# Optimization experiments

Measured on AMD Instinct MI355X. Metric: run time of the kernel, lower is better.

Reference implementation:

```python
import jax, jax.numpy as jnp
import numpy as np

B, S, D, H, OUT = 512, 200, 64, 512, 1
EPS = 1e-5  # torch LayerNorm default


def ln(x, g, b, axes=-1):
    m = x.mean(axis=axes, keepdims=True)
    v = ((x - m) ** 2).mean(axis=axes, keepdims=True)
    return (x - m) * jax.lax.rsqrt(v + EPS) * g + b


def lstm_layer(xs, W_ih, b_ih, W_hh, b_hh, g_ih, be_ih, g_hh, be_hh, g_ho, be_ho):
    # xs: (S, B, in_dim) -> (S, B, H)
    nb = xs.shape[1]
    def step(carry, x_t):
        h, c = carry
        gates = ln(x_t @ W_ih.T + b_ih, g_ih, be_ih) + ln(h @ W_hh.T + b_hh, g_hh, be_hh)
        i, f, g, o = jnp.split(gates, 4, axis=-1)
        c_new = jax.nn.sigmoid(f) * c + jax.nn.sigmoid(i) * jnp.tanh(g)
        h_new = jax.nn.sigmoid(o) * ln(jnp.tanh(c_new), g_ho, be_ho)
        return (h_new, c_new), h_new
    init = (jnp.zeros((nb, H), xs.dtype), jnp.zeros((nb, H), xs.dtype))
    _, hs = jax.lax.scan(step, init, xs)
    return hs


def setup_inputs() -> dict:
    key = jax.random.key(0)
    ks = iter(jax.random.split(key, 16))
    scale = 0.02
    def rn(shape):
        return jax.random.normal(next(ks), shape, jnp.float32) * scale
    inp = {"x": jax.random.normal(next(ks), (B, S, D), jnp.float32)}
    inp["ln1_g"] = jnp.ones((S, D), jnp.float32)
    inp["ln1_b"] = jnp.zeros((S, D), jnp.float32)
    for l, ind in ((0, D), (1, H)):
        inp[f"W_ih{l}"] = rn((4 * H, ind)); inp[f"b_ih{l}"] = jnp.zeros((4 * H,), jnp.float32)
        inp[f"W_hh{l}"] = rn((4 * H, H));  inp[f"b_hh{l}"] = jnp.zeros((4 * H,), jnp.float32)
        inp[f"g_ih{l}"] = jnp.ones((4 * H,), jnp.float32); inp[f"be_ih{l}"] = jnp.zeros((4 * H,), jnp.float32)
        inp[f"g_hh{l}"] = jnp.ones((4 * H,), jnp.float32); inp[f"be_hh{l}"] = jnp.zeros((4 * H,), jnp.float32)
        inp[f"g_ho{l}"] = jnp.ones((H,), jnp.float32);     inp[f"be_ho{l}"] = jnp.zeros((H,), jnp.float32)
    inp["Wd1"] = rn((H // 4, H));      inp["bd1"] = jnp.zeros((H // 4,), jnp.float32)
    inp["Wd2"] = rn((H // 8, H // 4)); inp["bd2"] = jnp.zeros((H // 8,), jnp.float32)
    inp["Wd3"] = rn((H // 16, H // 8)); inp["bd3"] = jnp.zeros((H // 16,), jnp.float32)
    inp["Wd4"] = rn((OUT, H // 16));   inp["bd4"] = jnp.zeros((OUT,), jnp.float32)
    return inp


def _forward(x, ln1_g, ln1_b,
             W_ih0, b_ih0, W_hh0, b_hh0, g_ih0, be_ih0, g_hh0, be_hh0, g_ho0, be_ho0,
             W_ih1, b_ih1, W_hh1, b_hh1, g_ih1, be_ih1, g_hh1, be_hh1, g_ho1, be_ho1,
             Wd1, bd1, Wd2, bd2, Wd3, bd3, Wd4, bd4):
    # ln1 normalizes jointly over (seq_len, input_dim)
    x = ln(x, ln1_g, ln1_b, axes=(-2, -1))
    xs = jnp.transpose(x, (1, 0, 2))  # (S, B, D)
    hs = lstm_layer(xs, W_ih0, b_ih0, W_hh0, b_hh0, g_ih0, be_ih0, g_hh0, be_hh0, g_ho0, be_ho0)
    hs = lstm_layer(hs, W_ih1, b_ih1, W_hh1, b_hh1, g_ih1, be_ih1, g_hh1, be_hh1, g_ho1, be_ho1)
    h_last = hs[-1]  # (B, H): last_num=1, eval-mode dropout is identity
    z = jax.nn.relu(h_last @ Wd1.T + bd1)
    z = jax.nn.relu(z @ Wd2.T + bd2)
    z = jax.nn.relu(z @ Wd3.T + bd3)
    return z @ Wd4.T + bd4  # (B, OUT)


def reference(x, ln1_g, ln1_b,
              W_ih0, b_ih0, W_hh0, b_hh0, g_ih0, be_ih0, g_hh0, be_hh0, g_ho0, be_ho0,
              W_ih1, b_ih1, W_hh1, b_hh1, g_ih1, be_ih1, g_hh1, be_hh1, g_ho1, be_ho1,
              Wd1, bd1, Wd2, bd2, Wd3, bd3, Wd4, bd4):
    return _forward(x, ln1_g, ln1_b,
                    W_ih0, b_ih0, W_hh0, b_hh0, g_ih0, be_ih0, g_hh0, be_hh0, g_ho0, be_ho0,
                    W_ih1, b_ih1, W_hh1, b_hh1, g_ih1, be_ih1, g_hh1, be_hh1, g_ho1, be_ho1,
                    Wd1, bd1, Wd2, bd2, Wd3, bd3, Wd4, bd4)
```

## Files before the change

kernel.cpp:

```cpp
#include <hip/hip_runtime.h>
#include <math.h>

#define BATCH 512
#define SEQ   200
#define DIN   64
#define HID   512
#define GW    2048
#define EPS   1e-5f
#define NREG  4

typedef _Float16 half_t;
typedef half_t half8 __attribute__((ext_vector_type(8)));
typedef float  f32x4  __attribute__((ext_vector_type(4)));
typedef float  f32x16 __attribute__((ext_vector_type(16)));

#define WN0 (2048*64)
#define WN1 (2048*512)
#define WTOT (WN0 + 3*WN1)
#define XFRAG ((size_t)SEQ*16*4*512)

__device__ __forceinline__ float sigf(float x){ return 1.0f/(1.0f+expf(-x)); }

__device__ __forceinline__ void gload16(const half_t* g, half_t* l){
  __builtin_amdgcn_global_load_lds(
      (const __attribute__((address_space(1))) void*)g,
      (__attribute__((address_space(3))) void*)l, 16, 0, 0);
}

__device__ __forceinline__ void barf(){
  asm volatile("" ::: "memory");
  __builtin_amdgcn_s_barrier();
  asm volatile("" ::: "memory");
}

__device__ __forceinline__ void block_reduce4(float&a,float&b,float&c,float&d,float* red){
  #pragma unroll
  for(int o=32;o;o>>=1){
    a+=__shfl_down(a,o); b+=__shfl_down(b,o);
    c+=__shfl_down(c,o); d+=__shfl_down(d,o);
  }
  const int lane = threadIdx.x & 63, wid = threadIdx.x>>6;
  if(lane==0){ red[wid*4+0]=a; red[wid*4+1]=b; red[wid*4+2]=c; red[wid*4+3]=d; }
  __syncthreads();
  a = red[0]+red[4]+red[8]+red[12];
  b = red[1]+red[5]+red[9]+red[13];
  c = red[2]+red[6]+red[10]+red[14];
  d = red[3]+red[7]+red[11]+red[15];
  __syncthreads();
}

__global__ __launch_bounds__(256) void ln1_stats(const float* __restrict__ x,
                                                 float* __restrict__ mu,
                                                 float* __restrict__ rs){
  const int b = blockIdx.x;
  const float* xb = x + (size_t)b*SEQ*DIN;
  float s=0, ss=0, d=0, e=0;
  for (int i=threadIdx.x; i<SEQ*DIN; i+=256){ float v=xb[i]; s+=v; ss+=v*v; }
  __shared__ float red[16];
  block_reduce4(s,ss,d,e,red);
  if (threadIdx.x==0){
    float m = s*(1.0f/(SEQ*DIN));
    mu[b] = m;
    rs[b] = rsqrtf(ss*(1.0f/(SEQ*DIN)) - m*m + EPS);
  }
}

__global__ __launch_bounds__(256) void wsplit(
    const float* __restrict__ W0, const float* __restrict__ W1,
    const float* __restrict__ W2, const float* __restrict__ W3,
    half_t* __restrict__ Wh, half_t* __restrict__ Wl)
{
  int i = blockIdx.x*256 + threadIdx.x;
  if (i >= WTOT) return;
  const float* src; int off, Kd;
  if (i < WN0){ src=W0; off=i; Kd=DIN; }
  else {
    int r = (i-WN0)/WN1; off = (i-WN0) - r*WN1; Kd=HID;
    src = (r==0)?W1:((r==1)?W2:W3);
  }
  const int C = Kd>>5;
  int j  = off & 7;
  int l  = (off>>3) & 63;
  int ks = (off>>9) & 1;
  int nf = (off>>10) & 1;
  int pc = off>>11;
  int c  = pc & (C-1);
  int p  = pc >> (Kd==DIN ? 1 : 4);
  int n  = p*64 + nf*32 + (l&31);
  int k  = c*32 + ks*16 + (l>>5)*8 + j;
  float v = src[(size_t)n*Kd + k];
  half_t h = (half_t)v;
  Wh[i] = h;
  Wl[i] = (half_t)(v - (float)h);
}

__global__ __launch_bounds__(256) void xprep(
    const float* __restrict__ x, const float* __restrict__ g1, const float* __restrict__ b1,
    const float* __restrict__ mu, const float* __restrict__ rs,
    half_t* __restrict__ xh, half_t* __restrict__ xl)
{
  size_t i = (size_t)blockIdx.x*256 + threadIdx.x;
  if (i >= XFRAG) return;
  int j   = (int)(i & 7);
  int l   = (int)((i>>3) & 63);
  int c   = (int)((i>>9) & 3);
  int mch = (int)((i>>11) & 15);
  int t   = (int)(i>>15);
  int b   = mch*32 + (l&31);
  int k   = c*16 + ((l>>5)<<3) + j;
  float v = (x[(size_t)b*(SEQ*DIN) + t*DIN + k] - mu[b]) * rs[b]
            * g1[t*DIN+k] + b1[t*DIN+k];
  half_t h = (half_t)v;
  xh[i] = h;
  xl[i] = (half_t)(v - (float)h);
}

__global__ __launch_bounds__(256, 1) void tick_mm64(
    const half_t* __restrict__ xh, const half_t* __restrict__ xl,
    const half_t* __restrict__ h0fh, const half_t* __restrict__ h0fl,
    const half_t* __restrict__ h1fh, const half_t* __restrict__ h1fl,
    const half_t* __restrict__ Wh, const half_t* __restrict__ Wl,
    float* __restrict__ G, int t)
{
  __shared__ half_t sbuf[2*16384];

  const int bi   = blockIdx.x;
  const int xcd  = bi & 7;
  const int slot = bi >> 3;
  const int z    = slot & 3;
  const int y    = (slot >> 2) & 3;
  const int x    = xcd*2 + (slot >> 4);

  const int tid  = threadIdx.x;
  const int lane = tid & 63;
  const int w    = tid >> 6;
  const int ln31 = lane & 31;

  const int mch0 = y*4 + (w>>1)*2;
  const int p    = x*2 + (w&1);
  const int wn0  = p*64;

  const half_t* BHb = Wh + WN0; const half_t* BLb = Wl + WN0;
  int Kd = HID;
  if (z==0){ BHb=Wh; BLb=Wl; Kd=DIN; }
  else if (z==2){ BHb=Wh+WN0+WN1; BLb=Wl+WN0+WN1; }
  else if (z==3){ BHb=Wh+WN0+2*WN1; BLb=Wl+WN0+2*WN1; }

  const int C32 = Kd >> 5;
  const int C16 = Kd >> 4;

  const int tq = (t < SEQ) ? t : (SEQ-1);
  const half_t *AHb, *ALb;
  if (z==0){ AHb = xh + (size_t)tq*32768; ALb = xl + (size_t)tq*32768; }
  else if (z==3){ AHb = h1fh; ALb = h1fl; }
  else { AHb = h0fh; ALb = h0fl; }

  auto stage = [&](int s){
    half_t* dst = sbuf + (size_t)(s&1)*16384;
    if (w < 2){
      #pragma unroll
      for (int q=0;q<2;q++){
        const int mci = w*2+q;
        const size_t abase = ((size_t)(y*4+mci)*C16 + 2*s)*512;
        #pragma unroll
        for (int pl=0;pl<2;pl++){
          const half_t* src = (pl? ALb : AHb) + abase + lane*8;
          half_t* d = dst + (mci*2+pl)*1024;
          gload16(src,       d);
          gload16(src + 512, d + 512);
        }
      }
    } else {
      const int ph = w-2;
      const size_t bbase = ((size_t)(x*2+ph)*C32 + s)*2048;
      #pragma unroll
      for (int pl=0;pl<2;pl++){
        const half_t* src = (pl? BLb : BHb) + bbase + lane*8;
        half_t* d = dst + 8192 + (ph*2+pl)*2048;
        #pragma unroll
        for (int i=0;i<4;i++)
          gload16(src + i*512, d + i*512);
      }
    }
  };

  f32x16 acc00 = {0.f,0.f,0.f,0.f,0.f,0.f,0.f,0.f,0.f,0.f,0.f,0.f,0.f,0.f,0.f,0.f};
  f32x16 acc01 = acc00, acc10 = acc00, acc11 = acc00;

  const int mh = w>>1, pw = w&1;
  auto compute = [&](const half_t* buf, int ks){
    const half_t* Ab = buf;
    const half_t* Bb = buf + 8192;
    half8 ah0 = *(const half8*)(Ab + ((mh*2+0)*2+0)*1024 + ks*512 + lane*8);
    half8 al0 = *(const half8*)(Ab + ((mh*2+0)*2+1)*1024 + ks*512 + lane*8);
    half8 ah1 = *(const half8*)(Ab + ((mh*2+1)*2+0)*1024 + ks*512 + lane*8);
    half8 al1 = *(const half8*)(Ab + ((mh*2+1)*2+1)*1024 + ks*512 + lane*8);
    half8 bh0 = *(const half8*)(Bb + ((pw*2+0)*4 + 0 + ks)*512 + lane*8);
    half8 bh1 = *(const half8*)(Bb + ((pw*2+0)*4 + 2 + ks)*512 + lane*8);
    half8 bl0 = *(const half8*)(Bb + ((pw*2+1)*4 + 0 + ks)*512 + lane*8);
    half8 bl1 = *(const half8*)(Bb + ((pw*2+1)*4 + 2 + ks)*512 + lane*8);
    acc00 = __builtin_amdgcn_mfma_f32_32x32x16_f16(ah0, bh0, acc00, 0,0,0);
    acc01 = __builtin_amdgcn_mfma_f32_32x32x16_f16(ah0, bh1, acc01, 0,0,0);
    acc10 = __builtin_amdgcn_mfma_f32_32x32x16_f16(ah1, bh0, acc10, 0,0,0);
    acc11 = __builtin_amdgcn_mfma_f32_32x32x16_f16(ah1, bh1, acc11, 0,0,0);
    acc00 = __builtin_amdgcn_mfma_f32_32x32x16_f16(al0, bh0, acc00, 0,0,0);
    acc01 = __builtin_amdgcn_mfma_f32_32x32x16_f16(al0, bh1, acc01, 0,0,0);
    acc10 = __builtin_amdgcn_mfma_f32_32x32x16_f16(al1, bh0, acc10, 0,0,0);
    acc11 = __builtin_amdgcn_mfma_f32_32x32x16_f16(al1, bh1, acc11, 0,0,0);
    acc00 = __builtin_amdgcn_mfma_f32_32x32x16_f16(ah0, bl0, acc00, 0,0,0);
    acc01 = __builtin_amdgcn_mfma_f32_32x32x16_f16(ah0, bl1, acc01, 0,0,0);
    acc10 = __builtin_amdgcn_mfma_f32_32x32x16_f16(ah1, bl0, acc10, 0,0,0);
    acc11 = __builtin_amdgcn_mfma_f32_32x32x16_f16(ah1, bl1, acc11, 0,0,0);
  };

  stage(0);
  for (int s=0; s<C32; ++s){
    if (s+1 < C32){
      stage(s+1);
      asm volatile("s_waitcnt vmcnt(8)" ::: "memory");
    } else {
      asm volatile("s_waitcnt vmcnt(0)" ::: "memory");
    }
    __builtin_amdgcn_sched_barrier(0);
    barf();
    const half_t* buf = sbuf + (size_t)(s&1)*16384;
    compute(buf, 0);
    compute(buf, 1);
    barf();
  }

  float* Gr = G + (size_t)z*BATCH*GW;
  const int rbase = (lane>>5)<<2;
  #pragma unroll
  for (int reg=0; reg<16; reg++){
    const int row = (reg&3) + ((reg>>2)<<3) + rbase;
    const int m0 = mch0*32 + row;
    const int m1 = m0 + 32;
    __builtin_nontemporal_store(acc00[reg], &Gr[(size_t)m0*GW + wn0 + ln31]);
    __builtin_nontemporal_store(acc01[reg], &Gr[(size_t)m0*GW + wn0 + 32 + ln31]);
    __builtin_nontemporal_store(acc10[reg], &Gr[(size_t)m1*GW + wn0 + ln31]);
    __builtin_nontemporal_store(acc11[reg], &Gr[(size_t)m1*GW + wn0 + 32 + ln31]);
  }
}

__global__ __launch_bounds__(256) void tick_update(
    const float* __restrict__ G,
    const float* __restrict__ b_ih0, const float* __restrict__ b_hh0,
    const float* __restrict__ b_ih1, const float* __restrict__ b_hh1,
    const float* __restrict__ g_ih0, const float* __restrict__ be_ih0,
    const float* __restrict__ g_hh0, const float* __restrict__ be_hh0,
    const float* __restrict__ g_ho0, const float* __restrict__ be_ho0,
    const float* __restrict__ g_ih1, const float* __restrict__ be_ih1,
    const float* __restrict__ g_hh1, const float* __restrict__ be_hh1,
    const float* __restrict__ g_ho1, const float* __restrict__ be_ho1,
    float* __restrict__ h0, float* __restrict__ c0,
    float* __restrict__ h1, float* __restrict__ c1,
    half_t* __restrict__ h0fh, half_t* __restrict__ h0fl,
    half_t* __restrict__ h1fh, half_t* __restrict__ h1fl, int t)
{
  const int layer = blockIdx.x >> 9;
  const int b = blockIdx.x & 511;
  if (layer==0 && t>=SEQ) return;
  if (layer==1 && t==0)   return;

  const float *GA,*GB,*bA,*bB,*gA,*beA,*gB,*beB,*gH,*bH;
  float *cs,*hs; half_t *hfx,*lfx;
  const size_t rb = (size_t)b*GW;
  if (layer==0){
    GA = G + rb;
    GB = G + (size_t)1*BATCH*GW + rb;
    bA=b_ih0; bB=b_hh0;
    gA=g_ih0; beA=be_ih0; gB=g_hh0; beB=be_hh0; gH=g_ho0; bH=be_ho0;
    cs = c0 + b*HID; hs = nullptr; hfx = h0fh; lfx = h0fl;
  } else {
    GA = G + (size_t)2*BATCH*GW + rb;
    GB = G + (size_t)3*BATCH*GW + rb;
    bA=b_ih1; bB=b_hh1;
    gA=g_ih1; beA=be_ih1; gB=g_hh1; beB=be_hh1; gH=g_ho1; bH=be_ho1;
    cs = c1 + b*HID; hs = (t==SEQ) ? (h1 + b*HID) : nullptr; hfx = h1fh; lfx = h1fl;
  }

  const int tid = threadIdx.x;
  __shared__ float red[16];
  __shared__ __align__(16) float GS[2*GW];
  __shared__ float su[HID];
  __shared__ float so[HID];

  float sa=0, ssa=0, sb=0, ssb=0;
  for (int i=tid*4; i<GW; i+=1024){
    f32x4 va = __builtin_nontemporal_load((const f32x4*)(GA+i));
    va += *(const f32x4*)(bA+i);
    *(f32x4*)(GS+i) = va;
    f32x4 vb = __builtin_nontemporal_load((const f32x4*)(GB+i));
    vb += *(const f32x4*)(bB+i);
    *(f32x4*)(GS+GW+i) = vb;
    #pragma unroll
    for (int q=0;q<4;q++){
      sa += va[q]; ssa += va[q]*va[q];
      sb += vb[q]; ssb += vb[q]*vb[q];
    }
  }
  block_reduce4(sa,ssa,sb,ssb,red);
  const float ma = sa*(1.0f/GW);
  const float ra = rsqrtf(ssa*(1.0f/GW) - ma*ma + EPS);
  const float mb = sb*(1.0f/GW);
  const float rb_ = rsqrtf(ssb*(1.0f/GW) - mb*mb + EPS);

  float s_u=0, s_uu=0;
  for (int j=tid;j<HID;j+=256){
    float iv = ((GS[j      ]-ma)*ra*gA[j      ]+beA[j      ]) + ((GS[GW+j      ]-mb)*rb_*gB[j      ]+beB[j      ]);
    float fv = ((GS[j+  HID]-ma)*ra*gA[j+  HID]+beA[j+  HID]) + ((GS[GW+j+  HID]-mb)*rb_*gB[j+  HID]+beB[j+  HID]);
    float gv = ((GS[j+2*HID]-ma)*ra*gA[j+2*HID]+beA[j+2*HID]) + ((GS[GW+j+2*HID]-mb)*rb_*gB[j+2*HID]+beB[j+2*HID]);
    float ov = ((GS[j+3*HID]-ma)*ra*gA[j+3*HID]+beA[j+3*HID]) + ((GS[GW+j+3*HID]-mb)*rb_*gB[j+3*HID]+beB[j+3*HID]);
    float cn = sigf(fv)*cs[j] + sigf(iv)*tanhf(gv);
    cs[j] = cn;
    float u = tanhf(cn);
    su[j] = u; so[j] = sigf(ov);
    s_u += u; s_uu += u*u;
  }
  float d3=0,d4=0;
  block_reduce4(s_u,s_uu,d3,d4,red);
  const float mu_u = s_u*(1.0f/HID);
  const float ru   = rsqrtf(s_uu*(1.0f/HID) - mu_u*mu_u + EPS);

  const size_t fbase = ((size_t)(b>>5)*32)*512 + (size_t)(b&31)*8;
  for (int j=tid;j<HID;j+=256){
    float v = so[j] * ((su[j]-mu_u)*ru*gH[j] + bH[j]);
    if (hs) hs[j] = v;
    half_t hv = (half_t)v;
    half_t lv = (half_t)(v - (float)hv);
    const size_t fi = fbase + (size_t)(j>>4)*512 + (size_t)((j>>3)&1)*256 + (j&7);
    hfx[fi] = hv;
    lfx[fi] = lv;
  }
}

__global__ __launch_bounds__(256) void head_kernel(
    const float* __restrict__ h1,
    const float* __restrict__ Wd1, const float* __restrict__ bd1,
    const float* __restrict__ Wd2, const float* __restrict__ bd2,
    const float* __restrict__ Wd3, const float* __restrict__ bd3,
    const float* __restrict__ Wd4, const float* __restrict__ bd4,
    float* __restrict__ out)
{
  const int b = blockIdx.x;
  __shared__ float hv[HID];
  __shared__ float z1[128];
  __shared__ float z2[64];
  __shared__ float z3[32];
  const int tid = threadIdx.x;
  for (int i=tid;i<HID;i+=256) hv[i]=h1[(size_t)b*HID+i];
  __syncthreads();
  if (tid<128){
    float acc=bd1[tid]; const float* w=Wd1+(size_t)tid*512;
    for(int k=0;k<512;k++) acc+=hv[k]*w[k];
    z1[tid]=fmaxf(acc,0.f);
  }
  __syncthreads();
  if (tid<64){
    float acc=bd2[tid]; const float* w=Wd2+(size_t)tid*128;
    for(int k=0;k<128;k++) acc+=z1[k]*w[k];
    z2[tid]=fmaxf(acc,0.f);
  }
  __syncthreads();
  if (tid<32){
    float acc=bd3[tid]; const float* w=Wd3+(size_t)tid*64;
    for(int k=0;k<64;k++) acc+=z2[k]*w[k];
    z3[tid]=fmaxf(acc,0.f);
  }
  __syncthreads();
  if (tid==0){
    float acc=bd4[0];
    for(int k=0;k<32;k++) acc+=z3[k]*Wd4[k];
    out[b]=acc;
  }
}

extern "C" void kernel_launch(void* const* d_in, const int* in_sizes, int n_in,
                              void* d_out, int out_size, void* d_ws, size_t ws_size,
                              hipStream_t stream) {
  const float* x      = (const float*)d_in[0];
  const float* ln1_g  = (const float*)d_in[1];
  const float* ln1_b  = (const float*)d_in[2];
  const float* W_ih0  = (const float*)d_in[3];
  const float* b_ih0  = (const float*)d_in[4];
  const float* W_hh0  = (const float*)d_in[5];
  const float* b_hh0  = (const float*)d_in[6];
  const float* g_ih0  = (const float*)d_in[7];
  const float* be_ih0 = (const float*)d_in[8];
  const float* g_hh0  = (const float*)d_in[9];
  const float* be_hh0 = (const float*)d_in[10];
  const float* g_ho0  = (const float*)d_in[11];
  const float* be_ho0 = (const float*)d_in[12];
  const float* W_ih1  = (const float*)d_in[13];
  const float* b_ih1  = (const float*)d_in[14];
  const float* W_hh1  = (const float*)d_in[15];
  const float* b_hh1  = (const float*)d_in[16];
  const float* g_ih1  = (const float*)d_in[17];
  const float* be_ih1 = (const float*)d_in[18];
  const float* g_hh1  = (const float*)d_in[19];
  const float* be_hh1 = (const float*)d_in[20];
  const float* g_ho1  = (const float*)d_in[21];
  const float* be_ho1 = (const float*)d_in[22];
  const float* Wd1    = (const float*)d_in[23];
  const float* bd1    = (const float*)d_in[24];
  const float* Wd2    = (const float*)d_in[25];
  const float* bd2    = (const float*)d_in[26];
  const float* Wd3    = (const float*)d_in[27];
  const float* bd3    = (const float*)d_in[28];
  const float* Wd4    = (const float*)d_in[29];
  const float* bd4    = (const float*)d_in[30];
  float* out = (float*)d_out;

  float* ws = (float*)d_ws;
  float* G  = ws;
  float* h0 = G  + NREG*(size_t)BATCH*GW;
  float* c0 = h0 + (size_t)BATCH*HID;
  float* h1 = c0 + (size_t)BATCH*HID;
  float* c1 = h1 + (size_t)BATCH*HID;
  half_t* h0fh = (half_t*)(c1 + (size_t)BATCH*HID);
  half_t* h0fl = h0fh + (size_t)BATCH*HID;
  half_t* h1fh = h0fl + (size_t)BATCH*HID;
  half_t* h1fl = h1fh + (size_t)BATCH*HID;
  float* mu = (float*)(h1fl + (size_t)BATCH*HID);
  float* rs = mu + BATCH;
  half_t* Wh = (half_t*)(rs + BATCH);
  half_t* Wl = Wh + (size_t)WTOT;
  half_t* xh = Wl + (size_t)WTOT;
  half_t* xl = xh + XFRAG;

  (void)hipMemsetAsync(h0, 0, 4*(size_t)BATCH*HID*4 + 4*(size_t)BATCH*HID*2, stream);

  ln1_stats<<<BATCH, 256, 0, stream>>>(x, mu, rs);
  wsplit<<<(WTOT+255)/256, 256, 0, stream>>>(W_ih0, W_hh0, W_ih1, W_hh1, Wh, Wl);
  xprep<<<(int)((XFRAG+255)/256), 256, 0, stream>>>(x, ln1_g, ln1_b, mu, rs, xh, xl);

  for (int t = 0; t <= SEQ; ++t) {
    tick_mm64<<<dim3(256), 256, 0, stream>>>(xh, xl,
        h0fh, h0fl, h1fh, h1fl, Wh, Wl, G, t);
    tick_update<<<dim3(1024), 256, 0, stream>>>(G,
        b_ih0, b_hh0, b_ih1, b_hh1,
        g_ih0, be_ih0, g_hh0, be_hh0, g_ho0, be_ho0,
        g_ih1, be_ih1, g_hh1, be_hh1, g_ho1, be_ho1,
        h0, c0, h1, c1, h0fh, h0fl, h1fh, h1fl, t);
  }
  head_kernel<<<BATCH, 256, 0, stream>>>(h1, Wd1, bd1, Wd2, bd2, Wd3, bd3, Wd4, bd4, out);
}
```

Before: 5.498 ms.

## Split K dimension of recurrent GEMMs across blocks and sum partials in update

The per-step GEMM kernel now launches 448 blocks instead of 256, giving each K=512 GEMM two blocks that each cover half of K, with the x-projection handled by a single block. The partial results go to seven separate G planes and the update kernel adds the two halves while loading them. Launch bounds are raised to allow two blocks per CU. The intent is to spread the short-K recurrent matmul across more CUs and cut per-step latency, at the cost of extra G memory traffic and an extra add in the update kernel.

Result: slower. 5.937 ms (+8.0%).

```diff
diff --git a/kernel.cpp b/kernel.cpp
--- a/kernel.cpp
+++ b/kernel.cpp
@@ -7,7 +7,7 @@
 #define HID   512
 #define GW    2048
 #define EPS   1e-5f
-#define NREG  4
+#define NREG  7
 
 typedef _Float16 half_t;
 typedef half_t half8 __attribute__((ext_vector_type(8)));
@@ -115,7 +115,7 @@
   xl[i] = (half_t)(v - (float)h);
 }
 
-__global__ __launch_bounds__(256, 1) void tick_mm64(
+__global__ __launch_bounds__(256, 2) void tick_mm64(
     const half_t* __restrict__ xh, const half_t* __restrict__ xl,
     const half_t* __restrict__ h0fh, const half_t* __restrict__ h0fl,
     const half_t* __restrict__ h1fh, const half_t* __restrict__ h1fl,
@@ -124,12 +124,13 @@
 {
   __shared__ half_t sbuf[2*16384];
 
-  const int bi   = blockIdx.x;
-  const int xcd  = bi & 7;
-  const int slot = bi >> 3;
-  const int z    = slot & 3;
-  const int y    = (slot >> 2) & 3;
-  const int x    = xcd*2 + (slot >> 4);
+  const int bi    = blockIdx.x;
+  const int zz    = bi >> 6;
+  const int which = (zz+1) >> 1;
+  const int kb    = zz ? ((zz-1)&1)*8 : 0;
+  const int ii    = bi & 63;
+  const int y     = ii & 3;
+  const int x     = ii >> 2;
 
   const int tid  = threadIdx.x;
   const int lane = tid & 63;
@@ -142,17 +143,18 @@
 
   const half_t* BHb = Wh + WN0; const half_t* BLb = Wl + WN0;
   int Kd = HID;
-  if (z==0){ BHb=Wh; BLb=Wl; Kd=DIN; }
-  else if (z==2){ BHb=Wh+WN0+WN1; BLb=Wl+WN0+WN1; }
-  else if (z==3){ BHb=Wh+WN0+2*WN1; BLb=Wl+WN0+2*WN1; }
-
-  const int C32 = Kd >> 5;
-  const int C16 = Kd >> 4;
+  if (which==0){ BHb=Wh; BLb=Wl; Kd=DIN; }
+  else if (which==2){ BHb=Wh+WN0+WN1; BLb=Wl+WN0+WN1; }
+  else if (which==3){ BHb=Wh+WN0+2*WN1; BLb=Wl+WN0+2*WN1; }
+
+  const int C32f = Kd >> 5;
+  const int C16f = Kd >> 4;
+  const int Cloc = (which==0) ? 2 : 8;
 
   const int tq = (t < SEQ) ? t : (SEQ-1);
   const half_t *AHb, *ALb;
-  if (z==0){ AHb = xh + (size_t)tq*32768; ALb = xl + (size_t)tq*32768; }
-  else if (z==3){ AHb = h1fh; ALb = h1fl; }
+  if (which==0){ AHb = xh + (size_t)tq*32768; ALb = xl + (size_t)tq*32768; }
+  else if (which==3){ AHb = h1fh; ALb = h1fl; }
   else { AHb = h0fh; ALb = h0fl; }
 
   auto stage = [&](int s){
@@ -161,7 +163,7 @@
       #pragma unroll
       for (int q=0;q<2;q++){
         const int mci = w*2+q;
-        const size_t abase = ((size_t)(y*4+mci)*C16 + 2*s)*512;
+        const size_t abase = ((size_t)(y*4+mci)*C16f + 2*(kb+s))*512;
         #pragma unroll
         for (int pl=0;pl<2;pl++){
           const half_t* src = (pl? ALb : AHb) + abase + lane*8;
@@ -172,7 +174,7 @@
       }
     } else {
       const int ph = w-2;
-      const size_t bbase = ((size_t)(x*2+ph)*C32 + s)*2048;
+      const size_t bbase = ((size_t)(x*2+ph)*C32f + kb + s)*2048;
       #pragma unroll
       for (int pl=0;pl<2;pl++){
         const half_t* src = (pl? BLb : BHb) + bbase + lane*8;
@@ -214,8 +216,8 @@
   };
 
   stage(0);
-  for (int s=0; s<C32; ++s){
-    if (s+1 < C32){
+  for (int s=0; s<Cloc; ++s){
+    if (s+1 < Cloc){
       stage(s+1);
       asm volatile("s_waitcnt vmcnt(8)" ::: "memory");
     } else {
@@ -229,7 +231,7 @@
     barf();
   }
 
-  float* Gr = G + (size_t)z*BATCH*GW;
+  float* Gr = G + (size_t)zz*BATCH*GW;
   const int rbase = (lane>>5)<<2;
   #pragma unroll
   for (int reg=0; reg<16; reg++){
@@ -263,18 +265,18 @@
   if (layer==0 && t>=SEQ) return;
   if (layer==1 && t==0)   return;
 
-  const float *GA,*GB,*bA,*bB,*gA,*beA,*gB,*beB,*gH,*bH;
+  const float *GA0,*GA1,*GB0,*GB1,*bA,*bB,*gA,*beA,*gB,*beB,*gH,*bH;
   float *cs,*hs; half_t *hfx,*lfx;
   const size_t rb = (size_t)b*GW;
   if (layer==0){
-    GA = G + rb;
-    GB = G + (size_t)1*BATCH*GW + rb;
+    GA0 = G + rb;                        GA1 = nullptr;
+    GB0 = G + (size_t)1*BATCH*GW + rb;   GB1 = G + (size_t)2*BATCH*GW + rb;
     bA=b_ih0; bB=b_hh0;
     gA=g_ih0; beA=be_ih0; gB=g_hh0; beB=be_hh0; gH=g_ho0; bH=be_ho0;
     cs = c0 + b*HID; hs = nullptr; hfx = h0fh; lfx = h0fl;
   } else {
-    GA = G + (size_t)2*BATCH*GW + rb;
-    GB = G + (size_t)3*BATCH*GW + rb;
+    GA0 = G + (size_t)3*BATCH*GW + rb;   GA1 = G + (size_t)4*BATCH*GW + rb;
+    GB0 = G + (size_t)5*BATCH*GW + rb;   GB1 = G + (size_t)6*BATCH*GW + rb;
     bA=b_ih1; bB=b_hh1;
     gA=g_ih1; beA=be_ih1; gB=g_hh1; beB=be_hh1; gH=g_ho1; bH=be_ho1;
     cs = c1 + b*HID; hs = (t==SEQ) ? (h1 + b*HID) : nullptr; hfx = h1fh; lfx = h1fl;
@@ -288,10 +290,12 @@
 
   float sa=0, ssa=0, sb=0, ssb=0;
   for (int i=tid*4; i<GW; i+=1024){
-    f32x4 va = __builtin_nontemporal_load((const f32x4*)(GA+i));
+    f32x4 va = __builtin_nontemporal_load((const f32x4*)(GA0+i));
+    if (GA1) va += __builtin_nontemporal_load((const f32x4*)(GA1+i));
     va += *(const f32x4*)(bA+i);
     *(f32x4*)(GS+i) = va;
-    f32x4 vb = __builtin_nontemporal_load((const f32x4*)(GB+i));
+    f32x4 vb = __builtin_nontemporal_load((const f32x4*)(GB0+i));
+    vb += __builtin_nontemporal_load((const f32x4*)(GB1+i));
     vb += *(const f32x4*)(bB+i);
     *(f32x4*)(GS+GW+i) = vb;
     #pragma unroll
@@ -436,7 +440,7 @@
   xprep<<<(int)((XFRAG+255)/256), 256, 0, stream>>>(x, ln1_g, ln1_b, mu, rs, xh, xl);
 
   for (int t = 0; t <= SEQ; ++t) {
-    tick_mm64<<<dim3(256), 256, 0, stream>>>(xh, xl,
+    tick_mm64<<<dim3(448), 256, 0, stream>>>(xh, xl,
         h0fh, h0fl, h1fh, h1fl, Wh, Wl, G, t);
     tick_update<<<dim3(1024), 256, 0, stream>>>(G,
         b_ih0, b_hh0, b_ih1, b_hh1,
```

## Fuse per-tick matmul and LSTM update into one kernel with grid barrier

Applied to the files above, without the earlier changes.

Merges the per-timestep MFMA gate matmul kernel and the LayerNorm/LSTM cell update kernel into a single launch. An atomic counter per tick acts as a grid-wide barrier between the two phases, which relies on all 256 blocks being co-resident. The update phase is remapped so each wave handles one (layer, batch) row, using wave shuffles instead of block reductions and reusing the matmul LDS buffer. This removes one kernel launch and its drain gap per timestep. The cost is a spin-wait barrier and only 1024 waves doing the elementwise update, far less parallelism than the previous 1024 blocks of 256 threads.

Measured after the change: 20.03 ms. 264% more time.

```diff
diff --git a/kernel.cpp b/kernel.cpp
--- a/kernel.cpp
+++ b/kernel.cpp
@@ -8,6 +8,7 @@
 #define GW    2048
 #define EPS   1e-5f
 #define NREG  4
+#define NBLK_MM 256
 
 typedef _Float16 half_t;
 typedef half_t half8 __attribute__((ext_vector_type(8)));
@@ -31,6 +32,18 @@
   asm volatile("" ::: "memory");
   __builtin_amdgcn_s_barrier();
   asm volatile("" ::: "memory");
+}
+
+__device__ __forceinline__ void wred2(float&a,float&b){
+  #pragma unroll
+  for(int o=32;o;o>>=1){ a+=__shfl_xor(a,o); b+=__shfl_xor(b,o); }
+}
+__device__ __forceinline__ void wred4(float&a,float&b,float&c,float&d){
+  #pragma unroll
+  for(int o=32;o;o>>=1){
+    a+=__shfl_xor(a,o); b+=__shfl_xor(b,o);
+    c+=__shfl_xor(c,o); d+=__shfl_xor(d,o);
+  }
 }
 
 __device__ __forceinline__ void block_reduce4(float&a,float&b,float&c,float&d,float* red){
@@ -115,136 +128,12 @@
   xl[i] = (half_t)(v - (float)h);
 }
 
-__global__ __launch_bounds__(256, 1) void tick_mm64(
+__global__ __launch_bounds__(256, 1) void tick_fused(
     const half_t* __restrict__ xh, const half_t* __restrict__ xl,
-    const half_t* __restrict__ h0fh, const half_t* __restrict__ h0fl,
-    const half_t* __restrict__ h1fh, const half_t* __restrict__ h1fl,
+    half_t* __restrict__ h0fh, half_t* __restrict__ h0fl,
+    half_t* __restrict__ h1fh, half_t* __restrict__ h1fl,
     const half_t* __restrict__ Wh, const half_t* __restrict__ Wl,
-    float* __restrict__ G, int t)
-{
-  __shared__ half_t sbuf[2*16384];
-
-  const int bi   = blockIdx.x;
-  const int xcd  = bi & 7;
-  const int slot = bi >> 3;
-  const int z    = slot & 3;
-  const int y    = (slot >> 2) & 3;
-  const int x    = xcd*2 + (slot >> 4);
-
-  const int tid  = threadIdx.x;
-  const int lane = tid & 63;
-  const int w    = tid >> 6;
-  const int ln31 = lane & 31;
-
-  const int mch0 = y*4 + (w>>1)*2;
-  const int p    = x*2 + (w&1);
-  const int wn0  = p*64;
-
-  const half_t* BHb = Wh + WN0; const half_t* BLb = Wl + WN0;
-  int Kd = HID;
-  if (z==0){ BHb=Wh; BLb=Wl; Kd=DIN; }
-  else if (z==2){ BHb=Wh+WN0+WN1; BLb=Wl+WN0+WN1; }
-  else if (z==3){ BHb=Wh+WN0+2*WN1; BLb=Wl+WN0+2*WN1; }
-
-  const int C32 = Kd >> 5;
-  const int C16 = Kd >> 4;
-
-  const int tq = (t < SEQ) ? t : (SEQ-1);
-  const half_t *AHb, *ALb;
-  if (z==0){ AHb = xh + (size_t)tq*32768; ALb = xl + (size_t)tq*32768; }
-  else if (z==3){ AHb = h1fh; ALb = h1fl; }
-  else { AHb = h0fh; ALb = h0fl; }
-
-  auto stage = [&](int s){
-    half_t* dst = sbuf + (size_t)(s&1)*16384;
-    if (w < 2){
-      #pragma unroll
-      for (int q=0;q<2;q++){
-        const int mci = w*2+q;
-        const size_t abase = ((size_t)(y*4+mci)*C16 + 2*s)*512;
-        #pragma unroll
-        for (int pl=0;pl<2;pl++){
-          const half_t* src = (pl? ALb : AHb) + abase + lane*8;
-          half_t* d = dst + (mci*2+pl)*1024;
-          gload16(src,       d);
-          gload16(src + 512, d + 512);
-        }
-      }
-    } else {
-      const int ph = w-2;
-      const size_t bbase = ((size_t)(x*2+ph)*C32 + s)*2048;
-      #pragma unroll
-      for (int pl=0;pl<2;pl++){
-        const half_t* src = (pl? BLb : BHb) + bbase + lane*8;
-        half_t* d = dst + 8192 + (ph*2+pl)*2048;
-        #pragma unroll
-        for (int i=0;i<4;i++)
-          gload16(src + i*512, d + i*512);
-      }
-    }
-  };
-
-  f32x16 acc00 = {0.f,0.f,0.f,0.f,0.f,0.f,0.f,0.f,0.f,0.f,0.f,0.f,0.f,0.f,0.f,0.f};
-  f32x16 acc01 = acc00, acc10 = acc00, acc11 = acc00;
-
-  const int mh = w>>1, pw = w&1;
-  auto compute = [&](const half_t* buf, int ks){
-    const half_t* Ab = buf;
-    const half_t* Bb = buf + 8192;
-    half8 ah0 = *(const half8*)(Ab + ((mh*2+0)*2+0)*1024 + ks*512 + lane*8);
-    half8 al0 = *(const half8*)(Ab + ((mh*2+0)*2+1)*1024 + ks*512 + lane*8);
-    half8 ah1 = *(const half8*)(Ab + ((mh*2+1)*2+0)*1024 + ks*512 + lane*8);
-    half8 al1 = *(const half8*)(Ab + ((mh*2+1)*2+1)*1024 + ks*512 + lane*8);
-    half8 bh0 = *(const half8*)(Bb + ((pw*2+0)*4 + 0 + ks)*512 + lane*8);
-    half8 bh1 = *(const half8*)(Bb + ((pw*2+0)*4 + 2 + ks)*512 + lane*8);
-    half8 bl0 = *(const half8*)(Bb + ((pw*2+1)*4 + 0 + ks)*512 + lane*8);
-    half8 bl1 = *(const half8*)(Bb + ((pw*2+1)*4 + 2 + ks)*512 + lane*8);
-    acc00 = __builtin_amdgcn_mfma_f32_32x32x16_f16(ah0, bh0, acc00, 0,0,0);
-    acc01 = __builtin_amdgcn_mfma_f32_32x32x16_f16(ah0, bh1, acc01, 0,0,0);
-    acc10 = __builtin_amdgcn_mfma_f32_32x32x16_f16(ah1, bh0, acc10, 0,0,0);
-    acc11 = __builtin_amdgcn_mfma_f32_32x32x16_f16(ah1, bh1, acc11, 0,0,0);
-    acc00 = __builtin_amdgcn_mfma_f32_32x32x16_f16(al0, bh0, acc00, 0,0,0);
-    acc01 = __builtin_amdgcn_mfma_f32_32x32x16_f16(al0, bh1, acc01, 0,0,0);
-    acc10 = __builtin_amdgcn_mfma_f32_32x32x16_f16(al1, bh0, acc10, 0,0,0);
-    acc11 = __builtin_amdgcn_mfma_f32_32x32x16_f16(al1, bh1, acc11, 0,0,0);
-    acc00 = __builtin_amdgcn_mfma_f32_32x32x16_f16(ah0, bl0, acc00, 0,0,0);
-    acc01 = __builtin_amdgcn_mfma_f32_32x32x16_f16(ah0, bl1, acc01, 0,0,0);
-    acc10 = __builtin_amdgcn_mfma_f32_32x32x16_f16(ah1, bl0, acc10, 0,0,0);
-    acc11 = __builtin_amdgcn_mfma_f32_32x32x16_f16(ah1, bl1, acc11, 0,0,0);
-  };
-
-  stage(0);
-  for (int s=0; s<C32; ++s){
-    if (s+1 < C32){
-      stage(s+1);
-      asm volatile("s_waitcnt vmcnt(8)" ::: "memory");
-    } else {
-      asm volatile("s_waitcnt vmcnt(0)" ::: "memory");
-    }
-    __builtin_amdgcn_sched_barrier(0);
-    barf();
-    const half_t* buf = sbuf + (size_t)(s&1)*16384;
-    compute(buf, 0);
-    compute(buf, 1);
-    barf();
-  }
-
-  float* Gr = G + (size_t)z*BATCH*GW;
-  const int rbase = (lane>>5)<<2;
-  #pragma unroll
-  for (int reg=0; reg<16; reg++){
-    const int row = (reg&3) + ((reg>>2)<<3) + rbase;
-    const int m0 = mch0*32 + row;
-    const int m1 = m0 + 32;
-    __builtin_nontemporal_store(acc00[reg], &Gr[(size_t)m0*GW + wn0 + ln31]);
-    __builtin_nontemporal_store(acc01[reg], &Gr[(size_t)m0*GW + wn0 + 32 + ln31]);
-    __builtin_nontemporal_store(acc10[reg], &Gr[(size_t)m1*GW + wn0 + ln31]);
-    __builtin_nontemporal_store(acc11[reg], &Gr[(size_t)m1*GW + wn0 + 32 + ln31]);
-  }
-}
-
-__global__ __launch_bounds__(256) void tick_update(
-    const float* __restrict__ G,
+    float* __restrict__ G, int* __restrict__ ctr,
     const float* __restrict__ b_ih0, const float* __restrict__ b_hh0,
     const float* __restrict__ b_ih1, const float* __restrict__ b_hh1,
     const float* __restrict__ g_ih0, const float* __restrict__ be_ih0,
@@ -253,85 +142,219 @@
     const float* __restrict__ g_ih1, const float* __restrict__ be_ih1,
     const float* __restrict__ g_hh1, const float* __restrict__ be_hh1,
     const float* __restrict__ g_ho1, const float* __restrict__ be_ho1,
-    float* __restrict__ h0, float* __restrict__ c0,
-    float* __restrict__ h1, float* __restrict__ c1,
-    half_t* __restrict__ h0fh, half_t* __restrict__ h0fl,
-    half_t* __restrict__ h1fh, half_t* __restrict__ h1fl, int t)
+    float* __restrict__ c0, float* __restrict__ c1, float* __restrict__ h1,
+    int t)
 {
-  const int layer = blockIdx.x >> 9;
-  const int b = blockIdx.x & 511;
-  if (layer==0 && t>=SEQ) return;
-  if (layer==1 && t==0)   return;
-
-  const float *GA,*GB,*bA,*bB,*gA,*beA,*gB,*beB,*gH,*bH;
-  float *cs,*hs; half_t *hfx,*lfx;
-  const size_t rb = (size_t)b*GW;
-  if (layer==0){
-    GA = G + rb;
-    GB = G + (size_t)1*BATCH*GW + rb;
-    bA=b_ih0; bB=b_hh0;
-    gA=g_ih0; beA=be_ih0; gB=g_hh0; beB=be_hh0; gH=g_ho0; bH=be_ho0;
-    cs = c0 + b*HID; hs = nullptr; hfx = h0fh; lfx = h0fl;
-  } else {
-    GA = G + (size_t)2*BATCH*GW + rb;
-    GB = G + (size_t)3*BATCH*GW + rb;
-    bA=b_ih1; bB=b_hh1;
-    gA=g_ih1; beA=be_ih1; gB=g_hh1; beB=be_hh1; gH=g_ho1; bH=be_ho1;
-    cs = c1 + b*HID; hs = (t==SEQ) ? (h1 + b*HID) : nullptr; hfx = h1fh; lfx = h1fl;
-  }
-
-  const int tid = threadIdx.x;
-  __shared__ float red[16];
-  __shared__ __align__(16) float GS[2*GW];
-  __shared__ float su[HID];
-  __shared__ float so[HID];
-
-  float sa=0, ssa=0, sb=0, ssb=0;
-  for (int i=tid*4; i<GW; i+=1024){
-    f32x4 va = __builtin_nontemporal_load((const f32x4*)(GA+i));
-    va += *(const f32x4*)(bA+i);
-    *(f32x4*)(GS+i) = va;
-    f32x4 vb = __builtin_nontemporal_load((const f32x4*)(GB+i));
-    vb += *(const f32x4*)(bB+i);
-    *(f32x4*)(GS+GW+i) = vb;
+  __shared__ __align__(16) half_t sbuf[2*16384];
+
+  const int bi   = blockIdx.x;
+  const int tid  = threadIdx.x;
+  const int lane = tid & 63;
+  const int w    = tid >> 6;
+  const int ln31 = lane & 31;
+
+  {
+    const int slot = bi >> 3;
+    const int z    = slot & 3;
+    const int y    = (slot >> 2) & 3;
+    const int x    = (bi & 7)*2 + (slot >> 4);
+
+    const int mch0 = y*4 + (w>>1)*2;
+    const int p    = x*2 + (w&1);
+    const int wn0  = p*64;
+
+    const half_t* BHb = Wh + WN0; const half_t* BLb = Wl + WN0;
+    int Kd = HID;
+    if (z==0){ BHb=Wh; BLb=Wl; Kd=DIN; }
+    else if (z==2){ BHb=Wh+WN0+WN1; BLb=Wl+WN0+WN1; }
+    else if (z==3){ BHb=Wh+WN0+2*WN1; BLb=Wl+WN0+2*WN1; }
+
+    const int C32 = Kd >> 5;
+    const int C16 = Kd >> 4;
+
+    const int tq = (t < SEQ) ? t : (SEQ-1);
+    const half_t *AHb, *ALb;
+    if (z==0){ AHb = xh + (size_t)tq*32768; ALb = xl + (size_t)tq*32768; }
+    else if (z==3){ AHb = h1fh; ALb = h1fl; }
+    else { AHb = h0fh; ALb = h0fl; }
+
+    auto stage = [&](int s){
+      half_t* dst = sbuf + (size_t)(s&1)*16384;
+      if (w < 2){
+        #pragma unroll
+        for (int q=0;q<2;q++){
+          const int mci = w*2+q;
+          const size_t abase = ((size_t)(y*4+mci)*C16 + 2*s)*512;
+          #pragma unroll
+          for (int pl=0;pl<2;pl++){
+            const half_t* src = (pl? ALb : AHb) + abase + lane*8;
+            half_t* d = dst + (mci*2+pl)*1024;
+            gload16(src,       d);
+            gload16(src + 512, d + 512);
+          }
+        }
+      } else {
+        const int ph = w-2;
+        const size_t bbase = ((size_t)(x*2+ph)*C32 + s)*2048;
+        #pragma unroll
+        for (int pl=0;pl<2;pl++){
+          const half_t* src = (pl? BLb : BHb) + bbase + lane*8;
+          half_t* d = dst + 8192 + (ph*2+pl)*2048;
+          #pragma unroll
+          for (int i=0;i<4;i++)
+            gload16(src + i*512, d + i*512);
+        }
+      }
+    };
+
+    f32x16 acc00 = {0.f,0.f,0.f,0.f,0.f,0.f,0.f,0.f,0.f,0.f,0.f,0.f,0.f,0.f,0.f,0.f};
+    f32x16 acc01 = acc00, acc10 = acc00, acc11 = acc00;
+
+    const int mh = w>>1, pw = w&1;
+    auto compute = [&](const half_t* buf, int ks){
+      const half_t* Ab = buf;
+      const half_t* Bb = buf + 8192;
+      half8 ah0 = *(const half8*)(Ab + ((mh*2+0)*2+0)*1024 + ks*512 + lane*8);
+      half8 al0 = *(const half8*)(Ab + ((mh*2+0)*2+1)*1024 + ks*512 + lane*8);
+      half8 ah1 = *(const half8*)(Ab + ((mh*2+1)*2+0)*1024 + ks*512 + lane*8);
+      half8 al1 = *(const half8*)(Ab + ((mh*2+1)*2+1)*1024 + ks*512 + lane*8);
+      half8 bh0 = *(const half8*)(Bb + ((pw*2+0)*4 + 0 + ks)*512 + lane*8);
+      half8 bh1 = *(const half8*)(Bb + ((pw*2+0)*4 + 2 + ks)*512 + lane*8);
+      half8 bl0 = *(const half8*)(Bb + ((pw*2+1)*4 + 0 + ks)*512 + lane*8);
+      half8 bl1 = *(const half8*)(Bb + ((pw*2+1)*4 + 2 + ks)*512 + lane*8);
+      acc00 = __builtin_amdgcn_mfma_f32_32x32x16_f16(ah0, bh0, acc00, 0,0,0);
+      acc01 = __builtin_amdgcn_mfma_f32_32x32x16_f16(ah0, bh1, acc01, 0,0,0);
+      acc10 = __builtin_amdgcn_mfma_f32_32x32x16_f16(ah1, bh0, acc10, 0,0,0);
+      acc11 = __builtin_amdgcn_mfma_f32_32x32x16_f16(ah1, bh1, acc11, 0,0,0);
+      acc00 = __builtin_amdgcn_mfma_f32_32x32x16_f16(al0, bh0, acc00, 0,0,0);
+      acc01 = __builtin_amdgcn_mfma_f32_32x32x16_f16(al0, bh1, acc01, 0,0,0);
+      acc10 = __builtin_amdgcn_mfma_f32_32x32x16_f16(al1, bh0, acc10, 0,0,0);
+      acc11 = __builtin_amdgcn_mfma_f32_32x32x16_f16(al1, bh1, acc11, 0,0,0);
+      acc00 = __builtin_amdgcn_mfma_f32_32x32x16_f16(ah0, bl0, acc00, 0,0,0);
+      acc01 = __builtin_amdgcn_mfma_f32_32x32x16_f16(ah0, bl1, acc01, 0,0,0);
+      acc10 = __builtin_amdgcn_mfma_f32_32x32x16_f16(ah1, bl0, acc10, 0,0,0);
+      acc11 = __builtin_amdgcn_mfma_f32_32x32x16_f16(ah1, bl1, acc11, 0,0,0);
+    };
+
+    stage(0);
+    for (int s=0; s<C32; ++s){
+      if (s+1 < C32){
+        stage(s+1);
+        asm volatile("s_waitcnt vmcnt(8)" ::: "memory");
+      } else {
+        asm volatile("s_waitcnt vmcnt(0)" ::: "memory");
+      }
+      __builtin_amdgcn_sched_barrier(0);
+      barf();
+      const half_t* buf = sbuf + (size_t)(s&1)*16384;
+      compute(buf, 0);
+      compute(buf, 1);
+      barf();
+    }
+
+    float* Gr = G + (size_t)z*BATCH*GW;
+    const int rbase = (lane>>5)<<2;
     #pragma unroll
-    for (int q=0;q<4;q++){
-      sa += va[q]; ssa += va[q]*va[q];
-      sb += vb[q]; ssb += vb[q]*vb[q];
-    }
-  }
-  block_reduce4(sa,ssa,sb,ssb,red);
-  const float ma = sa*(1.0f/GW);
-  const float ra = rsqrtf(ssa*(1.0f/GW) - ma*ma + EPS);
-  const float mb = sb*(1.0f/GW);
-  const float rb_ = rsqrtf(ssb*(1.0f/GW) - mb*mb + EPS);
-
-  float s_u=0, s_uu=0;
-  for (int j=tid;j<HID;j+=256){
-    float iv = ((GS[j      ]-ma)*ra*gA[j      ]+beA[j      ]) + ((GS[GW+j      ]-mb)*rb_*gB[j      ]+beB[j      ]);
-    float fv = ((GS[j+  HID]-ma)*ra*gA[j+  HID]+beA[j+  HID]) + ((GS[GW+j+  HID]-mb)*rb_*gB[j+  HID]+beB[j+  HID]);
-    float gv = ((GS[j+2*HID]-ma)*ra*gA[j+2*HID]+beA[j+2*HID]) + ((GS[GW+j+2*HID]-mb)*rb_*gB[j+2*HID]+beB[j+2*HID]);
-    float ov = ((GS[j+3*HID]-ma)*ra*gA[j+3*HID]+beA[j+3*HID]) + ((GS[GW+j+3*HID]-mb)*rb_*gB[j+3*HID]+beB[j+3*HID]);
-    float cn = sigf(fv)*cs[j] + sigf(iv)*tanhf(gv);
-    cs[j] = cn;
-    float u = tanhf(cn);
-    su[j] = u; so[j] = sigf(ov);
-    s_u += u; s_uu += u*u;
-  }
-  float d3=0,d4=0;
-  block_reduce4(s_u,s_uu,d3,d4,red);
-  const float mu_u = s_u*(1.0f/HID);
-  const float ru   = rsqrtf(s_uu*(1.0f/HID) - mu_u*mu_u + EPS);
-
-  const size_t fbase = ((size_t)(b>>5)*32)*512 + (size_t)(b&31)*8;
-  for (int j=tid;j<HID;j+=256){
-    float v = so[j] * ((su[j]-mu_u)*ru*gH[j] + bH[j]);
-    if (hs) hs[j] = v;
-    half_t hv = (half_t)v;
-    half_t lv = (half_t)(v - (float)hv);
-    const size_t fi = fbase + (size_t)(j>>4)*512 + (size_t)((j>>3)&1)*256 + (j&7);
-    hfx[fi] = hv;
-    lfx[fi] = lv;
+    for (int reg=0; reg<16; reg++){
+      const int row = (reg&3) + ((reg>>2)<<3) + rbase;
+      const int m0 = mch0*32 + row;
+      const int m1 = m0 + 32;
+      __builtin_nontemporal_store(acc00[reg], &Gr[(size_t)m0*GW + wn0 + ln31]);
+      __builtin_nontemporal_store(acc01[reg], &Gr[(size_t)m0*GW + wn0 + 32 + ln31]);
+      __builtin_nontemporal_store(acc10[reg], &Gr[(size_t)m1*GW + wn0 + ln31]);
+      __builtin_nontemporal_store(acc11[reg], &Gr[(size_t)m1*GW + wn0 + 32 + ln31]);
+    }
+  }
+
+  asm volatile("s_waitcnt vmcnt(0)" ::: "memory");
+  __threadfence();
+  __syncthreads();
+  if (tid==0){
+    __hip_atomic_fetch_add(&ctr[t], 1, __ATOMIC_RELEASE, __HIP_MEMORY_SCOPE_AGENT);
+    while (__hip_atomic_load(&ctr[t], __ATOMIC_ACQUIRE, __HIP_MEMORY_SCOPE_AGENT) < NBLK_MM)
+      __builtin_amdgcn_s_sleep(4);
+  }
+  __syncthreads();
+
+  {
+    const int unit  = w*256 + bi;
+    const int layer = unit >> 9;
+    const int b     = unit & 511;
+    const bool act  = (layer==0) ? (t < SEQ) : (t >= 1);
+    if (!act) return;
+
+    const float *GA,*GB,*bA,*bB,*gA,*beA,*gB,*beB,*gH,*bH;
+    float *cs, *hs=nullptr; half_t *hfx,*lfx;
+    const size_t rb = (size_t)b*GW;
+    if (layer==0){
+      GA = G + rb;
+      GB = G + (size_t)1*BATCH*GW + rb;
+      bA=b_ih0; bB=b_hh0;
+      gA=g_ih0; beA=be_ih0; gB=g_hh0; beB=be_hh0; gH=g_ho0; bH=be_ho0;
+      cs = c0 + b*HID; hfx = h0fh; lfx = h0fl;
+    } else {
+      GA = G + (size_t)2*BATCH*GW + rb;
+      GB = G + (size_t)3*BATCH*GW + rb;
+      bA=b_ih1; bB=b_hh1;
+      gA=g_ih1; beA=be_ih1; gB=g_hh1; beB=be_hh1; gH=g_ho1; bH=be_ho1;
+      cs = c1 + b*HID; hs = (t==SEQ) ? (h1 + b*HID) : nullptr; hfx = h1fh; lfx = h1fl;
+    }
+
+    float* GSw = ((float*)sbuf) + w*4096;
+
+    float sa=0, ssa=0, sb=0, ssb=0;
+    #pragma unroll
+    for (int q=0;q<8;q++){
+      const int i = q*256 + lane*4;
+      f32x4 va = __builtin_nontemporal_load((const f32x4*)(GA+i));
+      va += *(const f32x4*)(bA+i);
+      *(f32x4*)(GSw+i) = va;
+      f32x4 vb = __builtin_nontemporal_load((const f32x4*)(GB+i));
+      vb += *(const f32x4*)(bB+i);
+      *(f32x4*)(GSw+2048+i) = vb;
+      #pragma unroll
+      for (int q2=0;q2<4;q2++){
+        sa += va[q2]; ssa += va[q2]*va[q2];
+        sb += vb[q2]; ssb += vb[q2]*vb[q2];
+      }
+    }
+    wred4(sa,ssa,sb,ssb);
+    const float ma = sa*(1.0f/GW);
+    const float ra = rsqrtf(ssa*(1.0f/GW) - ma*ma + EPS);
+    const float mb2 = sb*(1.0f/GW);
+    const float rb2 = rsqrtf(ssb*(1.0f/GW) - mb2*mb2 + EPS);
+
+    float uu[8], oo[8];
+    float s_u=0, s_uu=0;
+    #pragma unroll
+    for (int q=0;q<8;q++){
+      const int j = q*64 + lane;
+      float iv = ((GSw[j      ]-ma)*ra*gA[j      ]+beA[j      ]) + ((GSw[2048+j      ]-mb2)*rb2*gB[j      ]+beB[j      ]);
+      float fv = ((GSw[j+  HID]-ma)*ra*gA[j+  HID]+beA[j+  HID]) + ((GSw[2048+j+  HID]-mb2)*rb2*gB[j+  HID]+beB[j+  HID]);
+      float gv = ((GSw[j+2*HID]-ma)*ra*gA[j+2*HID]+beA[j+2*HID]) + ((GSw[2048+j+2*HID]-mb2)*rb2*gB[j+2*HID]+beB[j+2*HID]);
+      float ov = ((GSw[j+3*HID]-ma)*ra*gA[j+3*HID]+beA[j+3*HID]) + ((GSw[2048+j+3*HID]-mb2)*rb2*gB[j+3*HID]+beB[j+3*HID]);
+      float cn = sigf(fv)*cs[j] + sigf(iv)*tanhf(gv);
+      cs[j] = cn;
+      float u = tanhf(cn);
+      uu[q] = u; oo[q] = sigf(ov);
+      s_u += u; s_uu += u*u;
+    }
+    wred2(s_u,s_uu);
+    const float mu_u = s_u*(1.0f/HID);
+    const float ru   = rsqrtf(s_uu*(1.0f/HID) - mu_u*mu_u + EPS);
+
+    const size_t fbase = ((size_t)(b>>5)*32)*512 + (size_t)(b&31)*8;
+    #pragma unroll
+    for (int q=0;q<8;q++){
+      const int j = q*64 + lane;
+      float v = oo[q] * ((uu[q]-mu_u)*ru*gH[j] + bH[j]);
+      if (hs) hs[j] = v;
+      half_t hv = (half_t)v;
+      half_t lv = (half_t)(v - (float)hv);
+      const size_t fi = fbase + (size_t)(j>>4)*512 + (size_t)((j>>3)&1)*256 + (j&7);
+      hfx[fi] = hv;
+      lfx[fi] = lv;
+    }
   }
 }
 
@@ -428,21 +451,22 @@
   half_t* Wl = Wh + (size_t)WTOT;
   half_t* xh = Wl + (size_t)WTOT;
   half_t* xl = xh + XFRAG;
+  int* ctr = (int*)(xl + XFRAG);
 
   (void)hipMemsetAsync(h0, 0, 4*(size_t)BATCH*HID*4 + 4*(size_t)BATCH*HID*2, stream);
+  (void)hipMemsetAsync(ctr, 0, 204*sizeof(int), stream);
 
   ln1_stats<<<BATCH, 256, 0, stream>>>(x, mu, rs);
   wsplit<<<(WTOT+255)/256, 256, 0, stream>>>(W_ih0, W_hh0, W_ih1, W_hh1, Wh, Wl);
   xprep<<<(int)((XFRAG+255)/256), 256, 0, stream>>>(x, ln1_g, ln1_b, mu, rs, xh, xl);
 
   for (int t = 0; t <= SEQ; ++t) {
-    tick_mm64<<<dim3(256), 256, 0, stream>>>(xh, xl,
-        h0fh, h0fl, h1fh, h1fl, Wh, Wl, G, t);
-    tick_update<<<dim3(1024), 256, 0, stream>>>(G,
+    tick_fused<<<dim3(NBLK_MM), 256, 0, stream>>>(xh, xl,
+        h0fh, h0fl, h1fh, h1fl, Wh, Wl, G, ctr,
         b_ih0, b_hh0, b_ih1, b_hh1,
         g_ih0, be_ih0, g_hh0, be_hh0, g_ho0, be_ho0,
         g_ih1, be_ih1, g_hh1, be_hh1, g_ho1, be_ho1,
-        h0, c0, h1, c1, h0fh, h0fl, h1fh, h1fl, t);
+        c0, c1, h1, t);
   }
   head_kernel<<<BATCH, 256, 0, stream>>>(h1, Wd1, bd1, Wd2, bd2, Wd3, bd3, Wd4, bd4, out);
 }
```
